# Kernel optimization log

Measured on AMD Instinct MI355X. Metric: run time of the kernel, lower is better.

Reference implementation:

```python
import jax, jax.numpy as jnp
import numpy as np

W_SIZE = 7      # number of windows per spatial dim (Wg = Hg)
CLUSTERS = 7    # adaptive-pool output per dim -> 49 centers per window


def _pool_matrix(in_size, out_size):
    # Row-stochastic matrix replicating torch AdaptiveAvgPool2d along one dim.
    P = np.zeros((out_size, in_size), dtype=np.float32)
    for i in range(out_size):
        s = (i * in_size) // out_size
        e = -((-(i + 1) * in_size) // out_size)  # ceil((i+1)*in/out)
        P[i, s:e] = 1.0 / (e - s)
    return jnp.asarray(P)


def _normalize(x, eps=1e-12):
    n = jnp.linalg.norm(x, axis=-1, keepdims=True)
    return x / jnp.maximum(n, eps)


def _forward(x_in, f_w, f_b, v_w, v_b, p_w, p_b, sim_alpha, sim_beta):
    B, C, H, W = x_in.shape
    Wg = Hg = W_SIZE
    w, h = H // Wg, W // Hg
    K = CLUSTERS * CLUSTERS  # 49 centers per window

    # 'b e (Wg w) (Hg h) -> (b Wg Hg) e w h'
    x = x_in.reshape(B, C, Wg, w, Hg, h).transpose(0, 2, 4, 1, 3, 5)
    x = x.reshape(B * Wg * Hg, C, w, h)
    x1, x2 = x[:, : C // 2], x[:, C // 2 :]

    # 1x1 convs f and v: dim//2 -> dim//16
    f = jnp.einsum('oc,bcwh->bowh', f_w, x1) + f_b[None, :, None, None]
    v = jnp.einsum('oc,bcwh->bowh', v_w, x2) + v_b[None, :, None, None]
    c = f.shape[1]

    Pw, Ph = _pool_matrix(w, CLUSTERS), _pool_matrix(h, CLUSTERS)
    # adaptive avg pool to (7,7)
    centers = jnp.einsum('iw,bcwh,jh->bcij', Pw, f, Ph)               # [Bw,c,7,7]
    value_centers = jnp.einsum('iw,bcwh,jh->bcij', Pw, v, Ph)
    value_centers = value_centers.reshape(-1, c, K).transpose(0, 2, 1)  # [Bw,K,c]

    cf = centers.reshape(-1, c, K).transpose(0, 2, 1)   # [Bw,K,c]
    ff = f.reshape(-1, c, w * h).transpose(0, 2, 1)      # [Bw,N,c]
    sim = jax.nn.sigmoid(
        sim_beta + sim_alpha * jnp.einsum('bmc,bnc->bmn', _normalize(cf), _normalize(ff))
    )  # [Bw,K,N]

    # hard assignment: each pixel attends only to its argmax center
    idx = jnp.argmax(sim, axis=1)                                   # [Bw,N]
    mask = (jnp.arange(K)[None, :, None] == idx[:, None, :]).astype(sim.dtype)
    sim = sim * mask

    v2 = v.reshape(-1, c, w * h).transpose(0, 2, 1)                 # [Bw,N,c]
    agg = (jnp.einsum('bmn,bnc->bmc', sim, v2) + value_centers) / (
        jnp.sum(sim, axis=-1, keepdims=True) + 1.0
    )                                                                # [Bw,K,c]
    out = jnp.einsum('bmn,bmc->bnc', sim, agg)                       # [Bw,N,c]

    out = out.transpose(0, 2, 1).reshape(-1, c, w, h)
    # '(b Wg Hg) e w h -> b e (Wg w) (Hg h)'
    out = out.reshape(B, Wg, Hg, c, w, h).transpose(0, 3, 1, 4, 2, 5)
    out = out.reshape(B, c, H, W)

    out = jnp.einsum('oc,bchw->bohw', p_w, out) + p_b[None, :, None, None]
    return out.reshape(B, out.shape[1], H * W)


def setup_inputs():
    key = jax.random.key(0)
    ks = jax.random.split(key, 4)
    B, dim, H, W = 16, 256, 112, 112
    c_in, c_mid = dim // 2, dim // 16
    s_f = 1.0 / np.sqrt(c_in)
    s_p = 1.0 / np.sqrt(c_mid)
    return {
        'x_in': jax.random.normal(ks[0], (B, dim, H, W), jnp.float32),
        'f_w': jax.random.normal(ks[1], (c_mid, c_in), jnp.float32) * s_f,
        'f_b': jnp.zeros((c_mid,), jnp.float32),
        'v_w': jax.random.normal(ks[2], (c_mid, c_in), jnp.float32) * s_f,
        'v_b': jnp.zeros((c_mid,), jnp.float32),
        'p_w': jax.random.normal(ks[3], (dim, c_mid), jnp.float32) * s_p,
        'p_b': jnp.zeros((dim,), jnp.float32),
        'sim_alpha': jnp.ones((1,), jnp.float32),
        'sim_beta': jnp.zeros((1,), jnp.float32),
    }


def reference(x_in, f_w, f_b, v_w, v_b, p_w, p_b, sim_alpha, sim_beta):
    return _forward(x_in, f_w, f_b, v_w, v_b, p_w, p_b, sim_alpha, sim_beta)
```

## Files before the change

kernel.cpp:

```cpp
#include <hip/hip_runtime.h>
#include <math.h>

#define HW 12544
#define IMW 112

#define GLOAD_LDS16(gp, lp) __builtin_amdgcn_global_load_lds( \
    (const __attribute__((address_space(1))) void*)(gp),      \
    (__attribute__((address_space(3))) void*)(lp), 16, 0, 0)

__device__ __forceinline__ float np_norm16(const float* a) {
    float q[16];
    #pragma unroll
    for (int i = 0; i < 16; ++i) q[i] = __fmul_rn(a[i], a[i]);
    float r0 = __fadd_rn(q[0], q[8]),  r1 = __fadd_rn(q[1], q[9]);
    float r2 = __fadd_rn(q[2], q[10]), r3 = __fadd_rn(q[3], q[11]);
    float r4 = __fadd_rn(q[4], q[12]), r5 = __fadd_rn(q[5], q[13]);
    float r6 = __fadd_rn(q[6], q[14]), r7 = __fadd_rn(q[7], q[15]);
    float s = __fadd_rn(__fadd_rn(__fadd_rn(r0, r1), __fadd_rn(r2, r3)),
                        __fadd_rn(__fadd_rn(r4, r5), __fadd_rn(r6, r7)));
    return fmaxf(__fsqrt_rn(s), 1e-12f);
}

__global__ __launch_bounds__(256, 4)
void lc_fused(const float* __restrict__ x,
              const float* __restrict__ fw, const float* __restrict__ fb,
              const float* __restrict__ vw, const float* __restrict__ vb,
              const float* __restrict__ pw, const float* __restrict__ pb,
              const float* __restrict__ alpha, const float* __restrict__ beta,
              float* __restrict__ out)
{
    __shared__ __attribute__((aligned(16))) float U[8192];
    __shared__ __attribute__((aligned(16))) float agg_s[784];
    __shared__ __attribute__((aligned(16))) float pb_s[256];
    __shared__ __attribute__((aligned(16))) float simv_s[256];
    __shared__ __attribute__((aligned(16))) int   bidx_s[256];

    float* fw_s    = U;
    float* vw_s    = U + 2048;
    float* xs      = U + 4096;
    float* f_s     = U;
    float* cent_s  = U + 4096;
    float* ncf_s   = U + 4880;
    float* vcent_s = U + 5664;
    float* simsum_s= U + 6448;
    float* Pagg_s  = U;

    const int t    = threadIdx.x;
    const int wave = t >> 6, lane = t & 63;
    const int py = t >> 4, px = t & 15;
    const int b  = blockIdx.x;
    const int batch = b / 49;
    const int rr = b % 49;
    const int gi = rr / 7, gj = rr % 7;
    const int row = gi*16 + py, col = gj*16 + px;

    for (int i = t; i < 512; i += 256) {
        ((float4*)fw_s)[i] = ((const float4*)fw)[i];
        ((float4*)vw_s)[i] = ((const float4*)vw)[i];
    }
    pb_s[t] = pb[t];
    for (int i = t; i < 784; i += 256) agg_s[i] = 0.f;

    const float* xbase = x + (size_t)batch*256*HW
                       + (size_t)(gi*16 + (lane >> 2))*IMW + gj*16 + (lane & 3)*4;

    float facc[16], vacc[16];
    #pragma unroll
    for (int o = 0; o < 16; ++o) { facc[o] = 0.f; vacc[o] = vb[o]; }

    for (int ch = 0; ch < 16; ++ch) {
        #pragma unroll
        for (int k = 0; k < 4; ++k) {
            const int sc = (wave << 2) + k;
            const int gc = (sc < 8) ? (ch*8 + sc)
                                    : (120 + ch*8 + sc);
            GLOAD_LDS16(xbase + (size_t)gc*HW, xs + (sc << 8));
        }
        __syncthreads();

        #pragma unroll
        for (int half = 0; half < 2; ++half) {
            const int c4 = (ch << 1) + half;
            const float* xf = xs + ((half*4) << 8) + t;
            const float* xv = xs + 2048 + ((half*4) << 8) + t;
            const float x0 = xf[0], x1 = xf[256], x2 = xf[512], x3 = xf[768];
            const float y0 = xv[0], y1 = xv[256], y2 = xv[512], y3 = xv[768];
            #pragma unroll
            for (int o = 0; o < 16; ++o) {
                const float* ar = fw_s + o*128 + c4*4;
                float s = facc[o];
                s = __fadd_rn(s, __fmul_rn(ar[0], x0));
                s = __fadd_rn(s, __fmul_rn(ar[1], x1));
                s = __fadd_rn(s, __fmul_rn(ar[2], x2));
                s = __fadd_rn(s, __fmul_rn(ar[3], x3));
                facc[o] = s;
                const float* cr = vw_s + o*128 + c4*4;
                vacc[o] = fmaf(cr[3], y3, fmaf(cr[2], y2, fmaf(cr[1], y1, fmaf(cr[0], y0, vacc[o]))));
            }
        }
        __syncthreads();
    }
    #pragma unroll
    for (int o = 0; o < 16; ++o) facc[o] = __fadd_rn(facc[o], fb[o]);

    for (int i = t; i < 784; i += 256) vcent_s[i] = 0.f;
    if (t < 49) simsum_s[t] = 0.f;
    __syncthreads();

    {
        float* fr = f_s + t*16;
        #pragma unroll
        for (int o = 0; o < 16; ++o) fr[o] = facc[o];
    }
    {
        const int   wss[7] = {0,2,4,6,9,11,13};
        const int   wee[7] = {3,5,7,10,12,14,16};
        const float wiv[7] = {1.f/3.f,1.f/3.f,1.f/3.f,0.25f,1.f/3.f,1.f/3.f,1.f/3.f};
        for (int i = 0; i < 7; ++i) {
            if (py < wss[i] || py >= wee[i]) continue;
            for (int j = 0; j < 7; ++j) {
                if (px < wss[j] || px >= wee[j]) continue;
                const float sc = wiv[i]*wiv[j];
                float* vb2 = vcent_s + (i*7+j)*16;
                #pragma unroll
                for (int o = 0; o < 16; ++o) atomicAdd(vb2 + o, vacc[o]*sc);
            }
        }
    }
    __syncthreads();

    {
        const int   wss[7] = {0,2,4,6,9,11,13};
        const int   wee[7] = {3,5,7,10,12,14,16};
        const float wiv[7] = {1.f/3.f,1.f/3.f,1.f/3.f,0.25f,1.f/3.f,1.f/3.f,1.f/3.f};
        for (int T = t; T < 784; T += 256) {
            int m = T >> 4, o = T & 15;
            int i = m / 7, j = m % 7;
            float pwv = wiv[i], phv = wiv[j];
            float s = 0.f;
            for (int r = wss[i]; r < wee[i]; ++r)
                for (int cc = wss[j]; cc < wee[j]; ++cc)
                    s = __fadd_rn(s, __fmul_rn(__fmul_rn(pwv, f_s[(r*16 + cc)*16 + o]), phv));
            cent_s[T] = s;
        }
    }
    __syncthreads();

    if (t < 49) {
        float rowv[16];
        #pragma unroll
        for (int o = 0; o < 16; ++o) rowv[o] = cent_s[t*16 + o];
        float n = np_norm16(rowv);
        #pragma unroll
        for (int o = 0; o < 16; ++o) ncf_s[t*16 + o] = __fdiv_rn(rowv[o], n);
    }
    __syncthreads();

    float nff[16];
    {
        float n = np_norm16(facc);
        #pragma unroll
        for (int o = 0; o < 16; ++o) nff[o] = __fdiv_rn(facc[o], n);
    }
    const float al = alpha[0], be = beta[0];
    float best = -1.0f; int bidx = 0;
    for (int m = 0; m < 49; ++m) {
        const float* cm = ncf_s + m*16;
        float s = 0.f;
        #pragma unroll
        for (int o = 0; o < 16; ++o) s = __fadd_rn(s, __fmul_rn(cm[o], nff[o]));
        float z = __fadd_rn(be, __fmul_rn(al, s));
        float sim = __fdiv_rn(1.0f, __fadd_rn(1.0f, expf(-z)));
        if (sim > best) { best = sim; bidx = m; }
    }
    const float simv = best;
    simv_s[t] = simv;
    bidx_s[t] = bidx;
    atomicAdd(&simsum_s[bidx], simv);
    {
        float* ab = agg_s + bidx*16;
        #pragma unroll
        for (int o = 0; o < 16; ++o) atomicAdd(ab + o, simv*vacc[o]);
    }
    __syncthreads();

    for (int T = t; T < 784; T += 256) {
        int m = T >> 4;
        agg_s[T] = (agg_s[T] + vcent_s[T]) / (simsum_s[m] + 1.0f);
    }
    __syncthreads();

    float* out_tile = out + (size_t)batch*256*HW + (size_t)(gi*16)*IMW + gj*16;
    float* op4 = out_tile + (lane >> 2)*IMW + (lane & 3)*4;
    const float4 sv4 = *(const float4*)(simv_s + (lane << 2));
    const int4   bi4 = *(const int4*)  (bidx_s + (lane << 2));

    const int oc6 = t >> 1;
    const int m0  = (t & 1) ? 25 : 0;
    const int m1  = (t & 1) ? 49 : 25;

    #pragma unroll
    for (int half = 0; half < 2; ++half) {
        {
            const int o = (half << 7) + oc6;
            const float4* pg = (const float4*)(pw + o*16);
            const float4 q0 = pg[0], q1 = pg[1], q2 = pg[2], q3 = pg[3];
            float* pr = Pagg_s + oc6*49;
            for (int m = m0; m < m1; ++m) {
                const float4* am = (const float4*)(agg_s + m*16);
                float4 a0 = am[0], a1 = am[1], a2 = am[2], a3 = am[3];
                float d;
                d = q0.x*a0.x;
                d = fmaf(q0.y,a0.y,d); d = fmaf(q0.z,a0.z,d); d = fmaf(q0.w,a0.w,d);
                d = fmaf(q1.x,a1.x,d); d = fmaf(q1.y,a1.y,d); d = fmaf(q1.z,a1.z,d);
                d = fmaf(q1.w,a1.w,d); d = fmaf(q2.x,a2.x,d); d = fmaf(q2.y,a2.y,d);
                d = fmaf(q2.z,a2.z,d); d = fmaf(q2.w,a2.w,d); d = fmaf(q3.x,a3.x,d);
                d = fmaf(q3.y,a3.y,d); d = fmaf(q3.z,a3.z,d); d = fmaf(q3.w,a3.w,d);
                pr[m] = d;
            }
        }
        __syncthreads();
        #pragma unroll 8
        for (int k = 0; k < 32; ++k) {
            const int oc = (wave << 5) + k;
            const int o  = (half << 7) + oc;
            const float* pr = Pagg_s + oc*49;
            const float pbo = pb_s[o];
            float4 r;
            r.x = fmaf(sv4.x, pr[bi4.x], pbo);
            r.y = fmaf(sv4.y, pr[bi4.y], pbo);
            r.z = fmaf(sv4.z, pr[bi4.z], pbo);
            r.w = fmaf(sv4.w, pr[bi4.w], pbo);
            *(float4*)(op4 + (size_t)o*HW) = r;
        }
        __syncthreads();
    }
}

extern "C" void kernel_launch(void* const* d_in, const int* in_sizes, int n_in,
                              void* d_out, int out_size, void* d_ws, size_t ws_size,
                              hipStream_t stream) {
    const float* x  = (const float*)d_in[0];
    const float* fw = (const float*)d_in[1];
    const float* fb = (const float*)d_in[2];
    const float* vw = (const float*)d_in[3];
    const float* vb = (const float*)d_in[4];
    const float* pw = (const float*)d_in[5];
    const float* pb = (const float*)d_in[6];
    const float* al = (const float*)d_in[7];
    const float* be = (const float*)d_in[8];
    float* out = (float*)d_out;

    dim3 grid(784), block(256);
    hipLaunchKernelGGL(lc_fused, grid, block, 0, stream,
                       x, fw, fb, vw, vb, pw, pb, al, be, out);
}
```

Before: 550.8 us.

## Split fused kernel into clustering kernel and wide output-projection kernel via workspace

Splits the single fused per-window kernel into two launches. The first computes the convs, centers, argmax assignment and aggregated values, and writes them to a workspace. The second runs 4x more blocks, each handling a quarter of the output channels, to spread the dominant output write across more CUs. The clustering kernel also drops the LDS async staging in favour of direct register loads with software prefetch. This adds an extra launch and a workspace round trip, and falls back to the fused kernel when no workspace is available.

New measurement: 555.5 us. No clear change (+0.9%).

```diff
diff --git a/kernel.cpp b/kernel.cpp
--- a/kernel.cpp
+++ b/kernel.cpp
@@ -19,6 +19,235 @@
     float s = __fadd_rn(__fadd_rn(__fadd_rn(r0, r1), __fadd_rn(r2, r3)),
                         __fadd_rn(__fadd_rn(r4, r5), __fadd_rn(r6, r7)));
     return fmaxf(__fsqrt_rn(s), 1e-12f);
+}
+
+__global__ __launch_bounds__(256, 4)
+void lc_cluster(const float* __restrict__ x,
+                const float* __restrict__ fw, const float* __restrict__ fb,
+                const float* __restrict__ vw, const float* __restrict__ vb,
+                const float* __restrict__ alpha, const float* __restrict__ beta,
+                float* __restrict__ aggws, float* __restrict__ simvws,
+                int* __restrict__ bidxws)
+{
+    __shared__ __attribute__((aligned(16))) float U[6656];
+    __shared__ __attribute__((aligned(16))) float agg_s[784];
+
+    float* fw_s    = U;
+    float* vw_s    = U + 2048;
+    float* f_s     = U;
+    float* cent_s  = U + 4096;
+    float* ncf_s   = U + 4880;
+    float* vcent_s = U + 5664;
+    float* simsum_s= U + 6448;
+
+    const int t  = threadIdx.x;
+    const int py = t >> 4, px = t & 15;
+    const int b  = blockIdx.x;
+    const int batch = b / 49;
+    const int rr = b % 49;
+    const int gi = rr / 7, gj = rr % 7;
+    const int row = gi*16 + py, col = gj*16 + px;
+
+    for (int i = t; i < 512; i += 256) {
+        ((float4*)fw_s)[i] = ((const float4*)fw)[i];
+        ((float4*)vw_s)[i] = ((const float4*)vw)[i];
+    }
+    for (int i = t; i < 784; i += 256) { vcent_s[i] = 0.f; agg_s[i] = 0.f; }
+    if (t < 49) simsum_s[t] = 0.f;
+    __syncthreads();
+
+    const float* xp = x + (size_t)batch*256*HW + (size_t)row*IMW + col;
+    const float* yp = xp + (size_t)128*HW;
+
+    float facc[16], vacc[16];
+    #pragma unroll
+    for (int o = 0; o < 16; ++o) { facc[o] = 0.f; vacc[o] = vb[o]; }
+
+    const float* xq = xp;
+    const float* yq = yp;
+    float xc0 = xq[0], xc1 = xq[HW], xc2 = xq[2*HW], xc3 = xq[3*HW];
+    float yc0 = yq[0], yc1 = yq[HW], yc2 = yq[2*HW], yc3 = yq[3*HW];
+
+    for (int c4 = 0; c4 < 32; ++c4) {
+        xq += 4*HW; yq += 4*HW;
+        float xn0, xn1, xn2, xn3, yn0, yn1, yn2, yn3;
+        if (c4 < 31) {
+            xn0 = xq[0]; xn1 = xq[HW]; xn2 = xq[2*HW]; xn3 = xq[3*HW];
+            yn0 = yq[0]; yn1 = yq[HW]; yn2 = yq[2*HW]; yn3 = yq[3*HW];
+        } else {
+            xn0 = xn1 = xn2 = xn3 = 0.f;
+            yn0 = yn1 = yn2 = yn3 = 0.f;
+        }
+        #pragma unroll
+        for (int o = 0; o < 16; ++o) {
+            const float* ar = fw_s + o*128 + c4*4;
+            float s = facc[o];
+            s = __fadd_rn(s, __fmul_rn(ar[0], xc0));
+            s = __fadd_rn(s, __fmul_rn(ar[1], xc1));
+            s = __fadd_rn(s, __fmul_rn(ar[2], xc2));
+            s = __fadd_rn(s, __fmul_rn(ar[3], xc3));
+            facc[o] = s;
+            const float* cr = vw_s + o*128 + c4*4;
+            vacc[o] = fmaf(cr[3], yc3, fmaf(cr[2], yc2, fmaf(cr[1], yc1, fmaf(cr[0], yc0, vacc[o]))));
+        }
+        xc0 = xn0; xc1 = xn1; xc2 = xn2; xc3 = xn3;
+        yc0 = yn0; yc1 = yn1; yc2 = yn2; yc3 = yn3;
+    }
+    #pragma unroll
+    for (int o = 0; o < 16; ++o) facc[o] = __fadd_rn(facc[o], fb[o]);
+
+    __syncthreads();
+
+    {
+        float* fr = f_s + t*16;
+        #pragma unroll
+        for (int o = 0; o < 16; ++o) fr[o] = facc[o];
+    }
+    {
+        const int   wss[7] = {0,2,4,6,9,11,13};
+        const int   wee[7] = {3,5,7,10,12,14,16};
+        const float wiv[7] = {1.f/3.f,1.f/3.f,1.f/3.f,0.25f,1.f/3.f,1.f/3.f,1.f/3.f};
+        for (int i = 0; i < 7; ++i) {
+            if (py < wss[i] || py >= wee[i]) continue;
+            for (int j = 0; j < 7; ++j) {
+                if (px < wss[j] || px >= wee[j]) continue;
+                const float sc = wiv[i]*wiv[j];
+                float* vb2 = vcent_s + (i*7+j)*16;
+                #pragma unroll
+                for (int o = 0; o < 16; ++o) atomicAdd(vb2 + o, vacc[o]*sc);
+            }
+        }
+    }
+    __syncthreads();
+
+    {
+        const int   wss[7] = {0,2,4,6,9,11,13};
+        const int   wee[7] = {3,5,7,10,12,14,16};
+        const float wiv[7] = {1.f/3.f,1.f/3.f,1.f/3.f,0.25f,1.f/3.f,1.f/3.f,1.f/3.f};
+        for (int T = t; T < 784; T += 256) {
+            int m = T >> 4, o = T & 15;
+            int i = m / 7, j = m % 7;
+            float pwv = wiv[i], phv = wiv[j];
+            float s = 0.f;
+            for (int r = wss[i]; r < wee[i]; ++r)
+                for (int cc = wss[j]; cc < wee[j]; ++cc)
+                    s = __fadd_rn(s, __fmul_rn(__fmul_rn(pwv, f_s[(r*16 + cc)*16 + o]), phv));
+            cent_s[T] = s;
+        }
+    }
+    __syncthreads();
+
+    if (t < 49) {
+        float rowv[16];
+        #pragma unroll
+        for (int o = 0; o < 16; ++o) rowv[o] = cent_s[t*16 + o];
+        float n = np_norm16(rowv);
+        #pragma unroll
+        for (int o = 0; o < 16; ++o) ncf_s[t*16 + o] = __fdiv_rn(rowv[o], n);
+    }
+    __syncthreads();
+
+    float nff[16];
+    {
+        float n = np_norm16(facc);
+        #pragma unroll
+        for (int o = 0; o < 16; ++o) nff[o] = __fdiv_rn(facc[o], n);
+    }
+    const float al = alpha[0], be = beta[0];
+    float best = -1.0f; int bidx = 0;
+    for (int m = 0; m < 49; ++m) {
+        const float* cm = ncf_s + m*16;
+        float s = 0.f;
+        #pragma unroll
+        for (int o = 0; o < 16; ++o) s = __fadd_rn(s, __fmul_rn(cm[o], nff[o]));
+        float z = __fadd_rn(be, __fmul_rn(al, s));
+        float sim = __fdiv_rn(1.0f, __fadd_rn(1.0f, expf(-z)));
+        if (sim > best) { best = sim; bidx = m; }
+    }
+    const float simv = best;
+    simvws[b*256 + t] = simv;
+    bidxws[b*256 + t] = bidx;
+    atomicAdd(&simsum_s[bidx], simv);
+    {
+        float* ab = agg_s + bidx*16;
+        #pragma unroll
+        for (int o = 0; o < 16; ++o) atomicAdd(ab + o, simv*vacc[o]);
+    }
+    __syncthreads();
+
+    for (int T = t; T < 784; T += 256) {
+        int m = T >> 4;
+        aggws[b*784 + T] = (agg_s[T] + vcent_s[T]) / (simsum_s[m] + 1.0f);
+    }
+}
+
+__global__ __launch_bounds__(256, 8)
+void lc_out(const float* __restrict__ pw, const float* __restrict__ pb,
+            const float* __restrict__ aggws, const float* __restrict__ simvws,
+            const int* __restrict__ bidxws, float* __restrict__ out)
+{
+    __shared__ __attribute__((aligned(16))) float agg_l[784];
+    __shared__ __attribute__((aligned(16))) float pw_l[1024];
+    __shared__ __attribute__((aligned(16))) float Pagg_l[64*49];
+    __shared__ __attribute__((aligned(16))) float simv_l[256];
+    __shared__ __attribute__((aligned(16))) int   bidx_l[256];
+    __shared__ __attribute__((aligned(16))) float pb_l[64];
+
+    const int t    = threadIdx.x;
+    const int wave = t >> 6, lane = t & 63;
+    const int bid  = blockIdx.x;
+    const int prob = bid >> 2, cg = bid & 3;
+    const int batch = prob / 49;
+    const int rr = prob % 49;
+    const int gi = rr / 7, gj = rr % 7;
+
+    for (int i = t; i < 784; i += 256) agg_l[i] = aggws[prob*784 + i];
+    for (int i = t; i < 1024; i += 256) pw_l[i] = pw[cg*1024 + i];
+    simv_l[t] = simvws[prob*256 + t];
+    bidx_l[t] = bidxws[prob*256 + t];
+    if (t < 64) pb_l[t] = pb[cg*64 + t];
+    __syncthreads();
+
+    {
+        const int oc_l = t >> 2, q = t & 3;
+        const int mq0[4] = {0,13,25,37};
+        const int mq1[4] = {13,25,37,49};
+        const float4* pg = (const float4*)(pw_l + oc_l*16);
+        const float4 q0 = pg[0], q1 = pg[1], q2 = pg[2], q3 = pg[3];
+        float* pr = Pagg_l + oc_l*49;
+        for (int m = mq0[q]; m < mq1[q]; ++m) {
+            const float4* am = (const float4*)(agg_l + m*16);
+            float4 a0 = am[0], a1 = am[1], a2 = am[2], a3 = am[3];
+            float d;
+            d = q0.x*a0.x;
+            d = fmaf(q0.y,a0.y,d); d = fmaf(q0.z,a0.z,d); d = fmaf(q0.w,a0.w,d);
+            d = fmaf(q1.x,a1.x,d); d = fmaf(q1.y,a1.y,d); d = fmaf(q1.z,a1.z,d);
+            d = fmaf(q1.w,a1.w,d); d = fmaf(q2.x,a2.x,d); d = fmaf(q2.y,a2.y,d);
+            d = fmaf(q2.z,a2.z,d); d = fmaf(q2.w,a2.w,d); d = fmaf(q3.x,a3.x,d);
+            d = fmaf(q3.y,a3.y,d); d = fmaf(q3.z,a3.z,d); d = fmaf(q3.w,a3.w,d);
+            pr[m] = d;
+        }
+    }
+    __syncthreads();
+
+    float* out_tile = out + (size_t)batch*256*HW + (size_t)(gi*16)*IMW + gj*16;
+    float* op4 = out_tile + (lane >> 2)*IMW + (lane & 3)*4;
+    const float4 sv4 = *(const float4*)(simv_l + (lane << 2));
+    const int4   bi4 = *(const int4*)  (bidx_l + (lane << 2));
+
+    #pragma unroll 8
+    for (int k = 0; k < 16; ++k) {
+        const int oc_l = (wave << 4) + k;
+        const int o    = (cg << 6) + oc_l;
+        const float* pr = Pagg_l + oc_l*49;
+        const float pbo = pb_l[oc_l];
+        float4 r;
+        r.x = fmaf(sv4.x, pr[bi4.x], pbo);
+        r.y = fmaf(sv4.y, pr[bi4.y], pbo);
+        r.z = fmaf(sv4.z, pr[bi4.z], pbo);
+        r.w = fmaf(sv4.w, pr[bi4.w], pbo);
+        *(float4*)(op4 + (size_t)o*HW) = r;
+    }
 }
 
 __global__ __launch_bounds__(256, 4)
@@ -52,7 +281,6 @@
     const int batch = b / 49;
     const int rr = b % 49;
     const int gi = rr / 7, gj = rr % 7;
-    const int row = gi*16 + py, col = gj*16 + px;
 
     for (int i = t; i < 512; i += 256) {
         ((float4*)fw_s)[i] = ((const float4*)fw)[i];
@@ -72,8 +300,7 @@
         #pragma unroll
         for (int k = 0; k < 4; ++k) {
             const int sc = (wave << 2) + k;
-            const int gc = (sc < 8) ? (ch*8 + sc)
-                                    : (120 + ch*8 + sc);
+            const int gc = (sc < 8) ? (ch*8 + sc) : (120 + ch*8 + sc);
             GLOAD_LDS16(xbase + (size_t)gc*HW, xs + (sc << 8));
         }
         __syncthreads();
@@ -251,7 +478,17 @@
     const float* be = (const float*)d_in[8];
     float* out = (float*)d_out;
 
-    dim3 grid(784), block(256);
-    hipLaunchKernelGGL(lc_fused, grid, block, 0, stream,
-                       x, fw, fb, vw, vb, pw, pb, al, be, out);
+    const size_t need = (size_t)784*784*4 + (size_t)784*256*4 + (size_t)784*256*4;
+    if (d_ws != nullptr && ws_size >= need) {
+        float* aggws  = (float*)d_ws;
+        float* simvws = aggws + (size_t)784*784;
+        int*   bidxws = (int*)(simvws + (size_t)784*256);
+        hipLaunchKernelGGL(lc_cluster, dim3(784), dim3(256), 0, stream,
+                           x, fw, fb, vw, vb, al, be, aggws, simvws, bidxws);
+        hipLaunchKernelGGL(lc_out, dim3(3136), dim3(256), 0, stream,
+                           pw, pb, aggws, simvws, bidxws, out);
+    } else {
+        hipLaunchKernelGGL(lc_fused, dim3(784), dim3(256), 0, stream,
+                           x, fw, fb, vw, vb, pw, pb, al, be, out);
+    }
 }
```
